# Performance work log

Hardware: AMD Instinct MI355X
Metric: run time of the kernel (lower is better)

The kernel has to match this reference:

```python
import jax, jax.numpy as jnp
import numpy as np

B, T, C_IN, CH, NRC, ED, NL, K = 16, 4096, 165, 256, 32, 64, 4, 512


def conv1x1(x, w, b):
    # x: [B,T,Cin], w: [Cout,Cin], b: [Cout]  (kernel-size-1 Conv1d == per-timestep matmul)
    return jnp.einsum('btc,oc->bto', x, w) + b


def resblock(x, wa, ba, wb, bb):
    h = jax.nn.relu(x)
    h = jax.nn.relu(conv1x1(h, wa, ba))
    h = conv1x1(h, wb, bb)
    return x + h


def quantize_level(res, embed):
    # res: [B,T,D], embed: [D,K]
    D = res.shape[-1]
    flat = res.reshape(-1, D)  # [N,D]
    dist = (flat * flat).sum(1, keepdims=True) - 2.0 * (flat @ embed) + (embed * embed).sum(0, keepdims=True)  # [N,K]
    ind = jnp.argmin(dist, axis=1)
    q = jnp.take(embed.T, ind, axis=0).reshape(res.shape)  # codebook gather
    diff = jnp.mean(jnp.square(jax.lax.stop_gradient(q) - res))
    q_st = res + jax.lax.stop_gradient(q - res)  # straight-through
    return q_st, diff


def _p(key, shape, fan_in):
    return jax.random.normal(key, shape, dtype=jnp.float32) / np.sqrt(fan_in)


def setup_inputs() -> dict:
    key = jax.random.key(0)
    ks = jax.random.split(key, 32)
    d = {
        'x': jax.random.normal(ks[0], (B, T, C_IN), dtype=jnp.float32),
        'enc_w1': _p(ks[1], (CH // 2, C_IN), C_IN), 'enc_b1': jnp.zeros((CH // 2,), jnp.float32),
        'enc_w2': _p(ks[2], (CH, CH // 2), CH // 2), 'enc_b2': jnp.zeros((CH,), jnp.float32),
        'enc_w3': _p(ks[3], (CH, CH), CH), 'enc_b3': jnp.zeros((CH,), jnp.float32),
        'enc_res_wa': _p(ks[4], (2, NRC, CH), CH), 'enc_res_ba': jnp.zeros((2, NRC), jnp.float32),
        'enc_res_wb': _p(ks[5], (2, CH, NRC), NRC), 'enc_res_bb': jnp.zeros((2, CH), jnp.float32),
        # quantize_conv: Conv(256->64)
        'q_w': _p(ks[6], (ED, CH), CH), 'q_b': jnp.zeros((ED,), jnp.float32),
        # 4 codebooks [D,K] (torch.randn init)
        'embeds': jax.random.normal(ks[7], (NL, ED, K), dtype=jnp.float32),
        'dec_w1': _p(ks[8], (CH, ED), ED), 'dec_b1': jnp.zeros((CH,), jnp.float32),
        'dec_res_wa': _p(ks[9], (2, NRC, CH), CH), 'dec_res_ba': jnp.zeros((2, NRC), jnp.float32),
        'dec_res_wb': _p(ks[10], (2, CH, NRC), NRC), 'dec_res_bb': jnp.zeros((2, CH), jnp.float32),
        'dec_w2': _p(ks[11], (CH // 2, CH), CH), 'dec_b2': jnp.zeros((CH // 2,), jnp.float32),
        'dec_w3': _p(ks[12], (C_IN, CH // 2), CH // 2), 'dec_b3': jnp.zeros((C_IN,), jnp.float32),
    }
    return d


def reference(x, enc_w1, enc_b1, enc_w2, enc_b2, enc_w3, enc_b3,
              enc_res_wa, enc_res_ba, enc_res_wb, enc_res_bb,
              q_w, q_b, embeds,
              dec_w1, dec_b1, dec_res_wa, dec_res_ba, dec_res_wb, dec_res_bb,
              dec_w2, dec_b2, dec_w3, dec_b3):
    # work entirely in [B,T,C] layout (transposes in the torch code cancel)
    h = jax.nn.relu(conv1x1(x, enc_w1, enc_b1))
    h = jax.nn.relu(conv1x1(h, enc_w2, enc_b2))
    h = conv1x1(h, enc_w3, enc_b3)
    for i in range(2):
        h = resblock(h, enc_res_wa[i], enc_res_ba[i], enc_res_wb[i], enc_res_bb[i])
    h = jax.nn.relu(h)
    quant = conv1x1(h, q_w, q_b)  # [B,T,64]

    residual = quant
    diffs = []
    main_q = None
    for i in range(NL):
        q, d = quantize_level(residual, embeds[i])
        diffs.append(d)
        residual = residual - q
        if i == 0:
            main_q = q
    diff = jnp.mean(jnp.stack(diffs))[None]  # shape [1]

    d = conv1x1(main_q, dec_w1, dec_b1)
    for i in range(2):
        d = resblock(d, dec_res_wa[i], dec_res_ba[i], dec_res_wb[i], dec_res_bb[i])
    d = jax.nn.relu(d)
    d = jax.nn.relu(conv1x1(d, dec_w2, dec_b2))
    d = conv1x1(d, dec_w3, dec_b3)  # [B,T,165]
    return d, diff
```

## Files before the change

kernel.cpp:

```cpp
#include <hip/hip_runtime.h>

#define NROWS 65536
#define SB 256

__device__ __forceinline__ float frelu(float v) { return fmaxf(v, 0.f); }

#define OFF_WT1   0
#define OFF_WT2   21504
#define OFF_WT3   54272
#define OFF_WTQ   119808
#define OFF_WTD1  136192
#define OFF_WTD2  152576
#define OFF_WTD3  185344
#define OFF_WAPE  218112
#define OFF_WBTE  234496
#define OFF_WAPD  250880
#define OFF_WBTD  267264
#define OFF_ETG   283648
#define OFF_EN2   414720
#define OFF_DSUM  416768
#define PREP_N    416769

__global__ void prep_k(const float* __restrict__ ew1, const float* __restrict__ ew2,
                       const float* __restrict__ ew3, const float* __restrict__ qw,
                       const float* __restrict__ dw1, const float* __restrict__ dw2,
                       const float* __restrict__ dw3, const float* __restrict__ ewa,
                       const float* __restrict__ ewb, const float* __restrict__ dwa,
                       const float* __restrict__ dwb, const float* __restrict__ embeds,
                       float* __restrict__ W) {
  int idx = blockIdx.x * 256 + threadIdx.x;
  if (idx < 21504) {
    int k = idx >> 7, o = idx & 127;
    W[OFF_WT1 + idx] = (k < 165) ? ew1[o * 165 + k] : 0.f;
    return;
  }
  idx -= 21504;
  if (idx < 32768) {
    int k = idx >> 8, o = idx & 255;
    W[OFF_WT2 + idx] = ew2[o * 128 + k];
    return;
  }
  idx -= 32768;
  if (idx < 65536) {
    int k = idx >> 8, o = idx & 255;
    W[OFF_WT3 + idx] = ew3[o * 256 + k];
    return;
  }
  idx -= 65536;
  if (idx < 16384) {
    int k = idx >> 6, o = idx & 63;
    W[OFF_WTQ + idx] = qw[o * 256 + k];
    return;
  }
  idx -= 16384;
  if (idx < 16384) {
    int k = idx >> 8, o = idx & 255;
    W[OFF_WTD1 + idx] = dw1[o * 64 + k];
    return;
  }
  idx -= 16384;
  if (idx < 32768) {
    int k = idx >> 7, o = idx & 127;
    W[OFF_WTD2 + idx] = dw2[o * 256 + k];
    return;
  }
  idx -= 32768;
  if (idx < 32768) {
    int k = idx >> 8, o = idx & 255;
    W[OFF_WTD3 + idx] = (o < 165) ? dw3[o * 128 + k] : 0.f;
    return;
  }
  idx -= 32768;
  if (idx < 16384) {
    int l = idx >> 13, rem = idx & 8191;
    int k4 = rem >> 7, rem2 = rem & 127, o = rem2 >> 2, kk = rem2 & 3;
    W[OFF_WAPE + idx] = ewa[l * 8192 + o * 256 + k4 * 4 + kk];
    return;
  }
  idx -= 16384;
  if (idx < 16384) {
    int l = idx >> 13, rem = idx & 8191;
    int k = rem >> 8, o = rem & 255;
    W[OFF_WBTE + idx] = ewb[l * 8192 + o * 32 + k];
    return;
  }
  idx -= 16384;
  if (idx < 16384) {
    int l = idx >> 13, rem = idx & 8191;
    int k4 = rem >> 7, rem2 = rem & 127, o = rem2 >> 2, kk = rem2 & 3;
    W[OFF_WAPD + idx] = dwa[l * 8192 + o * 256 + k4 * 4 + kk];
    return;
  }
  idx -= 16384;
  if (idx < 16384) {
    int l = idx >> 13, rem = idx & 8191;
    int k = rem >> 8, o = rem & 255;
    W[OFF_WBTD + idx] = dwb[l * 8192 + o * 32 + k];
    return;
  }
  idx -= 16384;
  if (idx < 131072) {
    int d = idx & 63, k = (idx >> 6) & 511, l = idx >> 15;
    W[OFF_ETG + idx] = embeds[(l * 64 + d) * 512 + k];
    return;
  }
  idx -= 131072;
  if (idx < 2048) {
    int l = idx >> 9, k = idx & 511;
    float s = 0.f;
    for (int d = 0; d < 64; ++d) {
      float e = embeds[(l * 64 + d) * 512 + k];
      s = fmaf(e, e, s);
    }
    W[OFF_EN2 + idx] = s;
    return;
  }
  idx -= 2048;
  if (idx == 0) W[OFF_DSUM] = 0.f;
}

template <int CIN, int CINP, int COUT, int CP, int INSTRIDE, int OUTSTRIDE, bool RELU_IN,
          bool RELU_OUT>
__global__ __launch_bounds__(256, 4) void conv2_k(const float* in, const float* __restrict__ wT,
                                                  const float* __restrict__ b, float* out) {
  constexpr int COUTP = 64 * CP;
  constexpr bool GUARD = (COUT != COUTP);
  typedef float vCP __attribute__((ext_vector_type(CP)));
  __shared__ float xs[32][CINP];
  const int tid = threadIdx.x, lane = tid & 63, wv = tid >> 6;
  const long row0 = (long)blockIdx.x * 32;

  for (int i = tid; i < 32 * CINP; i += 256) {
    const int r = i / CINP, c = i % CINP;
    float v = (CIN == CINP || c < CIN) ? in[(row0 + r) * (long)INSTRIDE + c] : 0.f;
    if (RELU_IN) v = frelu(v);
    xs[r][c] = v;
  }
  __syncthreads();

  float acc[8][CP];
#pragma unroll
  for (int i = 0; i < 8; ++i)
#pragma unroll
    for (int j = 0; j < CP; ++j) acc[i][j] = 0.f;

  const float* wbase = wT + lane * CP;
#pragma unroll 4
  for (int k0 = 0; k0 < CINP; k0 += 4) {
    vCP wk[4];
#pragma unroll
    for (int kk = 0; kk < 4; ++kk) wk[kk] = *(const vCP*)(wbase + (k0 + kk) * COUTP);
#pragma unroll
    for (int rj = 0; rj < 8; ++rj) {
      const float4 x = *(const float4*)(&xs[wv * 8 + rj][k0]);
#pragma unroll
      for (int j = 0; j < CP; ++j) {
        acc[rj][j] = fmaf(x.x, wk[0][j], acc[rj][j]);
        acc[rj][j] = fmaf(x.y, wk[1][j], acc[rj][j]);
        acc[rj][j] = fmaf(x.z, wk[2][j], acc[rj][j]);
        acc[rj][j] = fmaf(x.w, wk[3][j], acc[rj][j]);
      }
    }
  }

  float bias[CP];
#pragma unroll
  for (int j = 0; j < CP; ++j) {
    const int o = lane * CP + j;
    bias[j] = (!GUARD || o < COUT) ? b[o] : 0.f;
  }
#pragma unroll
  for (int rj = 0; rj < 8; ++rj) {
    const long rbase = (row0 + wv * 8 + rj) * (long)OUTSTRIDE;
    if constexpr (!GUARD) {
      vCP v;
#pragma unroll
      for (int j = 0; j < CP; ++j) {
        const float t = acc[rj][j] + bias[j];
        v[j] = RELU_OUT ? frelu(t) : t;
      }
      *(vCP*)(out + rbase + lane * CP) = v;
    } else {
#pragma unroll
      for (int j = 0; j < CP; ++j) {
        const int o = lane * CP + j;
        if (o < COUT) {
          const float t = acc[rj][j] + bias[j];
          out[rbase + o] = RELU_OUT ? frelu(t) : t;
        }
      }
    }
  }
}

template <int CIN, int COUT, int COUTP, int INSTRIDE, int OUTSTRIDE, bool RELU_IN, bool RELU_OUT>
__global__ __launch_bounds__(512, 2) void conv6_k(const float* __restrict__ in,
                                                  const float* __restrict__ wT,
                                                  const float* __restrict__ b,
                                                  float* __restrict__ out) {
  constexpr int MAXD = (CIN > COUT) ? CIN : COUT;
  __shared__ float lds[MAXD * 65];
  const int tid = threadIdx.x;
  const int lane = tid & 63;
  const int wv = __builtin_amdgcn_readfirstlane(tid >> 6);
  const long row0 = (long)blockIdx.x * 64;

  constexpr int C4 = CIN / 4;
  for (int i = tid; i < 64 * C4; i += 512) {
    const int r = i / C4, c4 = i % C4;
    float4 v = *(const float4*)(in + (row0 + r) * (long)INSTRIDE + c4 * 4);
    if (RELU_IN) {
      v.x = frelu(v.x);
      v.y = frelu(v.y);
      v.z = frelu(v.z);
      v.w = frelu(v.w);
    }
    lds[(c4 * 4 + 0) * 65 + r] = v.x;
    lds[(c4 * 4 + 1) * 65 + r] = v.y;
    lds[(c4 * 4 + 2) * 65 + r] = v.z;
    lds[(c4 * 4 + 3) * 65 + r] = v.w;
  }
  __syncthreads();

  float acc[32];
#pragma unroll
  for (int j = 0; j < 32; ++j) acc[j] = 0.f;

  const float* wrow = wT + wv * 32;
#pragma unroll 2
  for (int k = 0; k < CIN; ++k) {
    const float xv = lds[k * 65 + lane];
    const float* wk = wrow + (long)k * COUTP;
#pragma unroll
    for (int j = 0; j < 32; ++j) acc[j] = fmaf(xv, wk[j], acc[j]);
  }

  const float* bb = b + wv * 32;
#pragma unroll
  for (int j = 0; j < 32; ++j) {
    float t = acc[j] + bb[j];
    acc[j] = RELU_OUT ? frelu(t) : t;
  }

  __syncthreads();
#pragma unroll
  for (int j = 0; j < 32; ++j) lds[(wv * 32 + j) * 65 + lane] = acc[j];
  __syncthreads();

  constexpr int O4 = COUT / 4;
  for (int i = tid; i < 64 * O4; i += 512) {
    const int r = i / O4, c4 = i % O4;
    float4 v;
    v.x = lds[(c4 * 4 + 0) * 65 + r];
    v.y = lds[(c4 * 4 + 1) * 65 + r];
    v.z = lds[(c4 * 4 + 2) * 65 + r];
    v.w = lds[(c4 * 4 + 3) * 65 + r];
    *(float4*)(out + (row0 + r) * (long)OUTSTRIDE + c4 * 4) = v;
  }
}

__global__ __launch_bounds__(512, 4) void resblock_pair_k(
    float* xbuf, const float* __restrict__ waP, const float* __restrict__ ba,
    const float* __restrict__ wbT, const float* __restrict__ bb) {
  __shared__ float wls[8192];
  __shared__ float ts[64][36];
  const int tid = threadIdx.x, lane = tid & 63, wv = tid >> 6;
  const long row0 = (long)blockIdx.x * 64;
  const int o32 = lane & 31, rh = lane >> 5;

  for (int li = 0; li < 2; ++li) {
    __syncthreads();
    for (int i = tid; i < 8192; i += 512) wls[i] = waP[li * 8192 + i];
    __syncthreads();

    {
      float a0 = 0.f, a1 = 0.f, a2 = 0.f, a3 = 0.f;
      const float* xrow = xbuf + (row0 + wv * 8 + rh * 4) * (long)SB;
#pragma unroll 4
      for (int k0 = 0; k0 < 256; k0 += 4) {
        const float4 wq = *(const float4*)(&wls[k0 * 32 + o32 * 4]);
        const float4 x0 = *(const float4*)(xrow + 0 * SB + k0);
        const float4 x1 = *(const float4*)(xrow + 1 * SB + k0);
        const float4 x2 = *(const float4*)(xrow + 2 * SB + k0);
        const float4 x3 = *(const float4*)(xrow + 3 * SB + k0);
        a0 = fmaf(frelu(x0.x), wq.x, a0);
        a0 = fmaf(frelu(x0.y), wq.y, a0);
        a0 = fmaf(frelu(x0.z), wq.z, a0);
        a0 = fmaf(frelu(x0.w), wq.w, a0);
        a1 = fmaf(frelu(x1.x), wq.x, a1);
        a1 = fmaf(frelu(x1.y), wq.y, a1);
        a1 = fmaf(frelu(x1.z), wq.z, a1);
        a1 = fmaf(frelu(x1.w), wq.w, a1);
        a2 = fmaf(frelu(x2.x), wq.x, a2);
        a2 = fmaf(frelu(x2.y), wq.y, a2);
        a2 = fmaf(frelu(x2.z), wq.z, a2);
        a2 = fmaf(frelu(x2.w), wq.w, a2);
        a3 = fmaf(frelu(x3.x), wq.x, a3);
        a3 = fmaf(frelu(x3.y), wq.y, a3);
        a3 = fmaf(frelu(x3.z), wq.z, a3);
        a3 = fmaf(frelu(x3.w), wq.w, a3);
      }
      const float bal = ba[li * 32 + o32];
      const int rB = wv * 8 + rh * 4;
      ts[rB + 0][o32] = frelu(a0 + bal);
      ts[rB + 1][o32] = frelu(a1 + bal);
      ts[rB + 2][o32] = frelu(a2 + bal);
      ts[rB + 3][o32] = frelu(a3 + bal);
    }

    __syncthreads();
    for (int i = tid; i < 8192; i += 512) wls[i] = wbT[li * 8192 + i];
    __syncthreads();

    float acc2[8][4];
#pragma unroll
    for (int i = 0; i < 8; ++i)
#pragma unroll
      for (int j = 0; j < 4; ++j) acc2[i][j] = 0.f;

#pragma unroll
    for (int k0 = 0; k0 < 32; k0 += 4) {
      const float4 wk0 = *(const float4*)(&wls[(k0 + 0) * 256 + lane * 4]);
      const float4 wk1 = *(const float4*)(&wls[(k0 + 1) * 256 + lane * 4]);
      const float4 wk2 = *(const float4*)(&wls[(k0 + 2) * 256 + lane * 4]);
      const float4 wk3 = *(const float4*)(&wls[(k0 + 3) * 256 + lane * 4]);
#pragma unroll
      for (int rj = 0; rj < 8; ++rj) {
        const float4 t4 = *(const float4*)(&ts[wv * 8 + rj][k0]);
        acc2[rj][0] = fmaf(t4.x, wk0.x, acc2[rj][0]);
        acc2[rj][1] = fmaf(t4.x, wk0.y, acc2[rj][1]);
        acc2[rj][2] = fmaf(t4.x, wk0.z, acc2[rj][2]);
        acc2[rj][3] = fmaf(t4.x, wk0.w, acc2[rj][3]);
        acc2[rj][0] = fmaf(t4.y, wk1.x, acc2[rj][0]);
        acc2[rj][1] = fmaf(t4.y, wk1.y, acc2[rj][1]);
        acc2[rj][2] = fmaf(t4.y, wk1.z, acc2[rj][2]);
        acc2[rj][3] = fmaf(t4.y, wk1.w, acc2[rj][3]);
        acc2[rj][0] = fmaf(t4.z, wk2.x, acc2[rj][0]);
        acc2[rj][1] = fmaf(t4.z, wk2.y, acc2[rj][1]);
        acc2[rj][2] = fmaf(t4.z, wk2.z, acc2[rj][2]);
        acc2[rj][3] = fmaf(t4.z, wk2.w, acc2[rj][3]);
        acc2[rj][0] = fmaf(t4.w, wk3.x, acc2[rj][0]);
        acc2[rj][1] = fmaf(t4.w, wk3.y, acc2[rj][1]);
        acc2[rj][2] = fmaf(t4.w, wk3.z, acc2[rj][2]);
        acc2[rj][3] = fmaf(t4.w, wk3.w, acc2[rj][3]);
      }
    }
    const float4 bbv = *(const float4*)(bb + li * 256 + lane * 4);
#pragma unroll
    for (int rj = 0; rj < 8; ++rj) {
      float* xp = xbuf + (row0 + wv * 8 + rj) * (long)SB + lane * 4;
      const float4 xv = *(const float4*)xp;
      float4 nv;
      nv.x = xv.x + acc2[rj][0] + bbv.x;
      nv.y = xv.y + acc2[rj][1] + bbv.y;
      nv.z = xv.z + acc2[rj][2] + bbv.z;
      nv.w = xv.w + acc2[rj][3] + bbv.w;
      *(float4*)xp = nv;
    }
  }
}

__global__ __launch_bounds__(256, 3) void vq_fused_k(
    float* buf, const float* __restrict__ wTq, const float* __restrict__ qb,
    const float* __restrict__ embeds, const float* __restrict__ en2,
    const float* __restrict__ etg, float* __restrict__ dsum,
    const float* __restrict__ wTd1, const float* __restrict__ d1b) {
  __shared__ float xs[32][256];
  __shared__ float resL[32][68];
  __shared__ float mq[32][68];
  const int tid = threadIdx.x;
  const int lane = tid & 63;
  const int wv = tid >> 6;
  const long row0 = (long)blockIdx.x * 32;

  for (int i = tid; i < 32 * 256; i += 256) {
    const int r = i >> 8, c = i & 255;
    xs[r][c] = frelu(buf[(row0 + r) * (long)SB + c]);
  }
  __syncthreads();

  {
    float qacc[8];
#pragma unroll
    for (int i = 0; i < 8; ++i) qacc[i] = 0.f;
#pragma unroll 2
    for (int k0 = 0; k0 < 256; k0 += 4) {
      const float w0 = wTq[(k0 + 0) * 64 + lane];
      const float w1 = wTq[(k0 + 1) * 64 + lane];
      const float w2 = wTq[(k0 + 2) * 64 + lane];
      const float w3 = wTq[(k0 + 3) * 64 + lane];
#pragma unroll
      for (int rj = 0; rj < 8; ++rj) {
        const float4 x = *(const float4*)(&xs[wv * 8 + rj][k0]);
        qacc[rj] = fmaf(x.x, w0, qacc[rj]);
        qacc[rj] = fmaf(x.y, w1, qacc[rj]);
        qacc[rj] = fmaf(x.z, w2, qacc[rj]);
        qacc[rj] = fmaf(x.w, w3, qacc[rj]);
      }
    }
    const float qbv = qb[lane];
#pragma unroll
    for (int rj = 0; rj < 8; ++rj) resL[wv * 8 + rj][lane] = qacc[rj] + qbv;
  }

  float dloc = 0.f;

  for (int l = 0; l < 4; ++l) {
    float best[8];
    int bk[8];
#pragma unroll
    for (int i = 0; i < 8; ++i) {
      best[i] = 3.4e38f;
      bk[i] = 0;
    }

    for (int kc = 0; kc < 2; ++kc) {
      float acc[8][4];
#pragma unroll
      for (int i = 0; i < 8; ++i)
#pragma unroll
        for (int j = 0; j < 4; ++j) acc[i][j] = 0.f;

      const float* eb = embeds + ((long)l << 15) + (kc << 8) + lane * 4;
#pragma unroll 2
      for (int dq = 0; dq < 16; ++dq) {
        float4 x4[8];
#pragma unroll
        for (int rj = 0; rj < 8; ++rj) x4[rj] = *(const float4*)(&resL[wv * 8 + rj][dq * 4]);
#pragma unroll
        for (int dd = 0; dd < 4; ++dd) {
          const float4 e4 = *(const float4*)(eb + ((dq * 4 + dd) << 9));
#pragma unroll
          for (int rj = 0; rj < 8; ++rj) {
            const float xv = dd == 0 ? x4[rj].x : dd == 1 ? x4[rj].y : dd == 2 ? x4[rj].z : x4[rj].w;
            acc[rj][0] = fmaf(xv, e4.x, acc[rj][0]);
            acc[rj][1] = fmaf(xv, e4.y, acc[rj][1]);
            acc[rj][2] = fmaf(xv, e4.z, acc[rj][2]);
            acc[rj][3] = fmaf(xv, e4.w, acc[rj][3]);
          }
        }
      }

      const float4 e2 = *(const float4*)(en2 + l * 512 + kc * 256 + lane * 4);
#pragma unroll
      for (int rj = 0; rj < 8; ++rj) {
#pragma unroll
        for (int j = 0; j < 4; ++j) {
          const float ev = j == 0 ? e2.x : j == 1 ? e2.y : j == 2 ? e2.z : e2.w;
          const float s = fmaf(-2.f, acc[rj][j], ev);
          const int k = kc * 256 + lane * 4 + j;
          if (s < best[rj]) {
            best[rj] = s;
            bk[rj] = k;
          }
        }
      }
    }

#pragma unroll
    for (int rj = 0; rj < 8; ++rj) {
      float bv = best[rj];
      int bi = bk[rj];
#pragma unroll
      for (int m = 1; m < 64; m <<= 1) {
        const float ov = __shfl_xor(bv, m, 64);
        const int ok = __shfl_xor(bi, m, 64);
        if (ov < bv || (ov == bv && ok < bi)) {
          bv = ov;
          bi = ok;
        }
      }
      bk[rj] = bi;
    }

#pragma unroll
    for (int rj = 0; rj < 8; ++rj) {
      const int r = wv * 8 + rj;
      const float q = etg[((long)((l << 9) + bk[rj])) * 64 + lane];
      const float res = resL[r][lane];
      const float t = q - res;
      const float qst = res + t;
      dloc = fmaf(t, t, dloc);
      resL[r][lane] = res - qst;
      if (l == 0) mq[r][lane] = qst;
    }
  }

#pragma unroll
  for (int m = 1; m < 64; m <<= 1) dloc += __shfl_xor(dloc, m, 64);
  if (lane == 0) atomicAdd(dsum, dloc);

  {
    float acc1[8][4];
#pragma unroll
    for (int i = 0; i < 8; ++i)
#pragma unroll
      for (int j = 0; j < 4; ++j) acc1[i][j] = 0.f;

    const float* w1base = wTd1 + lane * 4;
#pragma unroll 2
    for (int d = 0; d < 64; d += 2) {
      const float4 wA = *(const float4*)(w1base + (d + 0) * 256);
      const float4 wB = *(const float4*)(w1base + (d + 1) * 256);
#pragma unroll
      for (int rj = 0; rj < 8; ++rj) {
        const int r = wv * 8 + rj;
        const float xA = mq[r][d];
        const float xB = mq[r][d + 1];
        acc1[rj][0] = fmaf(xA, wA.x, acc1[rj][0]);
        acc1[rj][1] = fmaf(xA, wA.y, acc1[rj][1]);
        acc1[rj][2] = fmaf(xA, wA.z, acc1[rj][2]);
        acc1[rj][3] = fmaf(xA, wA.w, acc1[rj][3]);
        acc1[rj][0] = fmaf(xB, wB.x, acc1[rj][0]);
        acc1[rj][1] = fmaf(xB, wB.y, acc1[rj][1]);
        acc1[rj][2] = fmaf(xB, wB.z, acc1[rj][2]);
        acc1[rj][3] = fmaf(xB, wB.w, acc1[rj][3]);
      }
    }
    const float4 bv = *(const float4*)(d1b + lane * 4);
#pragma unroll
    for (int rj = 0; rj < 8; ++rj) {
      float4 v;
      v.x = acc1[rj][0] + bv.x;
      v.y = acc1[rj][1] + bv.y;
      v.z = acc1[rj][2] + bv.z;
      v.w = acc1[rj][3] + bv.w;
      *(float4*)(buf + (row0 + wv * 8 + rj) * (long)SB + lane * 4) = v;
    }
  }
}

__global__ __launch_bounds__(256, 3) void dec23_k(const float* __restrict__ in,
                                                  const float* __restrict__ wTd2,
                                                  const float* __restrict__ b2,
                                                  const float* __restrict__ wTd3,
                                                  const float* __restrict__ b3,
                                                  float* __restrict__ out) {
  __shared__ float xs[32][256];
  __shared__ float ts[32][132];
  const int tid = threadIdx.x, lane = tid & 63, wv = tid >> 6;
  const long row0 = (long)blockIdx.x * 32;

  for (int i = tid; i < 32 * 256; i += 256) {
    const int r = i >> 8, c = i & 255;
    xs[r][c] = frelu(in[(row0 + r) * (long)SB + c]);
  }
  __syncthreads();

  {
    float a2[8][2];
#pragma unroll
    for (int i = 0; i < 8; ++i) {
      a2[i][0] = 0.f;
      a2[i][1] = 0.f;
    }
    const float* w2base = wTd2 + lane * 2;
#pragma unroll 2
    for (int k0 = 0; k0 < 256; k0 += 4) {
      const float2 w0 = *(const float2*)(w2base + (k0 + 0) * 128);
      const float2 w1 = *(const float2*)(w2base + (k0 + 1) * 128);
      const float2 w2v = *(const float2*)(w2base + (k0 + 2) * 128);
      const float2 w3 = *(const float2*)(w2base + (k0 + 3) * 128);
#pragma unroll
      for (int rj = 0; rj < 8; ++rj) {
        const float4 x = *(const float4*)(&xs[wv * 8 + rj][k0]);
        a2[rj][0] = fmaf(x.x, w0.x, a2[rj][0]);
        a2[rj][1] = fmaf(x.x, w0.y, a2[rj][1]);
        a2[rj][0] = fmaf(x.y, w1.x, a2[rj][0]);
        a2[rj][1] = fmaf(x.y, w1.y, a2[rj][1]);
        a2[rj][0] = fmaf(x.z, w2v.x, a2[rj][0]);
        a2[rj][1] = fmaf(x.z, w2v.y, a2[rj][1]);
        a2[rj][0] = fmaf(x.w, w3.x, a2[rj][0]);
        a2[rj][1] = fmaf(x.w, w3.y, a2[rj][1]);
      }
    }
    const float b20 = b2[lane * 2 + 0];
    const float b21 = b2[lane * 2 + 1];
#pragma unroll
    for (int rj = 0; rj < 8; ++rj) {
      const int r = wv * 8 + rj;
      ts[r][lane * 2 + 0] = frelu(a2[rj][0] + b20);
      ts[r][lane * 2 + 1] = frelu(a2[rj][1] + b21);
    }
  }

  {
    float a3[8][4];
#pragma unroll
    for (int i = 0; i < 8; ++i)
#pragma unroll
      for (int j = 0; j < 4; ++j) a3[i][j] = 0.f;

    const float* w3base = wTd3 + lane * 4;
#pragma unroll 2
    for (int k0 = 0; k0 < 128; k0 += 4) {
      const float4 wk0 = *(const float4*)(w3base + (k0 + 0) * 256);
      const float4 wk1 = *(const float4*)(w3base + (k0 + 1) * 256);
      const float4 wk2 = *(const float4*)(w3base + (k0 + 2) * 256);
      const float4 wk3 = *(const float4*)(w3base + (k0 + 3) * 256);
#pragma unroll
      for (int rj = 0; rj < 8; ++rj) {
        const float4 t4 = *(const float4*)(&ts[wv * 8 + rj][k0]);
        a3[rj][0] = fmaf(t4.x, wk0.x, a3[rj][0]);
        a3[rj][1] = fmaf(t4.x, wk0.y, a3[rj][1]);
        a3[rj][2] = fmaf(t4.x, wk0.z, a3[rj][2]);
        a3[rj][3] = fmaf(t4.x, wk0.w, a3[rj][3]);
        a3[rj][0] = fmaf(t4.y, wk1.x, a3[rj][0]);
        a3[rj][1] = fmaf(t4.y, wk1.y, a3[rj][1]);
        a3[rj][2] = fmaf(t4.y, wk1.z, a3[rj][2]);
        a3[rj][3] = fmaf(t4.y, wk1.w, a3[rj][3]);
        a3[rj][0] = fmaf(t4.z, wk2.x, a3[rj][0]);
        a3[rj][1] = fmaf(t4.z, wk2.y, a3[rj][1]);
        a3[rj][2] = fmaf(t4.z, wk2.z, a3[rj][2]);
        a3[rj][3] = fmaf(t4.z, wk2.w, a3[rj][3]);
        a3[rj][0] = fmaf(t4.w, wk3.x, a3[rj][0]);
        a3[rj][1] = fmaf(t4.w, wk3.y, a3[rj][1]);
        a3[rj][2] = fmaf(t4.w, wk3.z, a3[rj][2]);
        a3[rj][3] = fmaf(t4.w, wk3.w, a3[rj][3]);
      }
    }
    float bias[4];
#pragma unroll
    for (int j = 0; j < 4; ++j) {
      const int o = lane * 4 + j;
      bias[j] = (o < 165) ? b3[o] : 0.f;
    }
#pragma unroll
    for (int rj = 0; rj < 8; ++rj) {
      const long rbase = (row0 + wv * 8 + rj) * 165L;
#pragma unroll
      for (int j = 0; j < 4; ++j) {
        const int o = lane * 4 + j;
        if (o < 165) out[rbase + o] = a3[rj][j] + bias[j];
      }
    }
  }
}

__global__ void finalize_k(const float* __restrict__ dsum, float* __restrict__ out) {
  if (threadIdx.x == 0 && blockIdx.x == 0)
    out[0] = *dsum * (1.0f / (4.0f * 65536.0f * 64.0f));
}

extern "C" void kernel_launch(void* const* d_in, const int* in_sizes, int n_in, void* d_out,
                              int out_size, void* d_ws, size_t ws_size, hipStream_t stream) {
  (void)in_sizes; (void)n_in; (void)out_size; (void)ws_size;
  const float* x = (const float*)d_in[0];
  const float* enc_w1 = (const float*)d_in[1];
  const float* enc_b1 = (const float*)d_in[2];
  const float* enc_w2 = (const float*)d_in[3];
  const float* enc_b2 = (const float*)d_in[4];
  const float* enc_w3 = (const float*)d_in[5];
  const float* enc_b3 = (const float*)d_in[6];
  const float* enc_res_wa = (const float*)d_in[7];
  const float* enc_res_ba = (const float*)d_in[8];
  const float* enc_res_wb = (const float*)d_in[9];
  const float* enc_res_bb = (const float*)d_in[10];
  const float* q_w = (const float*)d_in[11];
  const float* q_b = (const float*)d_in[12];
  const float* embeds = (const float*)d_in[13];
  const float* dec_w1 = (const float*)d_in[14];
  const float* dec_b1 = (const float*)d_in[15];
  const float* dec_res_wa = (const float*)d_in[16];
  const float* dec_res_ba = (const float*)d_in[17];
  const float* dec_res_wb = (const float*)d_in[18];
  const float* dec_res_bb = (const float*)d_in[19];
  const float* dec_w2 = (const float*)d_in[20];
  const float* dec_b2 = (const float*)d_in[21];
  const float* dec_w3 = (const float*)d_in[22];
  const float* dec_b3 = (const float*)d_in[23];

  float* ws = (float*)d_ws;
  float* buf = ws;
  float* W = ws + (long)NROWS * SB;

  float* dout = (float*)d_out;

  prep_k<<<(PREP_N + 255) / 256, 256, 0, stream>>>(enc_w1, enc_w2, enc_w3, q_w, dec_w1, dec_w2,
                                                   dec_w3, enc_res_wa, enc_res_wb, dec_res_wa,
                                                   dec_res_wb, embeds, W);

  const int GB = NROWS / 32;
  const int GR = NROWS / 64;

  conv2_k<165, 168, 128, 2, 165, SB, false, true><<<GB, 256, 0, stream>>>(x, W + OFF_WT1, enc_b1, buf);
  conv6_k<128, 256, 256, SB, SB, false, true><<<GR, 512, 0, stream>>>(buf, W + OFF_WT2, enc_b2, buf);
  conv6_k<256, 256, 256, SB, SB, false, false><<<GR, 512, 0, stream>>>(buf, W + OFF_WT3, enc_b3, buf);
  resblock_pair_k<<<GR, 512, 0, stream>>>(buf, W + OFF_WAPE, enc_res_ba, W + OFF_WBTE, enc_res_bb);

  vq_fused_k<<<GB, 256, 0, stream>>>(buf, W + OFF_WTQ, q_b, embeds, W + OFF_EN2, W + OFF_ETG,
                                     W + OFF_DSUM, W + OFF_WTD1, dec_b1);

  resblock_pair_k<<<GR, 512, 0, stream>>>(buf, W + OFF_WAPD, dec_res_ba, W + OFF_WBTD, dec_res_bb);
  dec23_k<<<GB, 256, 0, stream>>>(buf, W + OFF_WTD2, dec_b2, W + OFF_WTD3, dec_b3, dout);

  finalize_k<<<1, 64, 0, stream>>>(W + OFF_DSUM, dout + (long)NROWS * 165);
}
```

Before: 1.171 ms.

## Restructure fused VQ kernel to hold residual rows in registers

Rewrites the fused quantize kernel so that each lane keeps one row's 64-dim residual in registers. Each of the four waves scans a quarter of the codebook through row-major, wave-uniform (broadcast) reads, and the per-wave winners are combined through LDS. Blocks now cover 64 rows with 256 threads and read the encoder activations straight from global memory instead of staging them in LDS. The scalar dot-product loop is meant to cut LDS traffic and shuffle reductions, at the cost of 64+ live registers per lane, lower occupancy (launch bounds of 2), and an argmin tie-break that no longer explicitly prefers the lower index across waves.

```diff
diff --git a/kernel.cpp b/kernel.cpp
--- a/kernel.cpp
+++ b/kernel.cpp
@@ -360,29 +360,23 @@
   }
 }
 
-__global__ __launch_bounds__(256, 3) void vq_fused_k(
+__global__ __launch_bounds__(256, 2) void vq8_k(
     float* buf, const float* __restrict__ wTq, const float* __restrict__ qb,
-    const float* __restrict__ embeds, const float* __restrict__ en2,
-    const float* __restrict__ etg, float* __restrict__ dsum,
-    const float* __restrict__ wTd1, const float* __restrict__ d1b) {
-  __shared__ float xs[32][256];
-  __shared__ float resL[32][68];
-  __shared__ float mq[32][68];
-  const int tid = threadIdx.x;
-  const int lane = tid & 63;
-  const int wv = tid >> 6;
-  const long row0 = (long)blockIdx.x * 32;
-
-  for (int i = tid; i < 32 * 256; i += 256) {
-    const int r = i >> 8, c = i & 255;
-    xs[r][c] = frelu(buf[(row0 + r) * (long)SB + c]);
-  }
-  __syncthreads();
+    const float* __restrict__ en2, const float* __restrict__ etg,
+    float* __restrict__ dsum, const float* __restrict__ wTd1, const float* __restrict__ d1b) {
+  __shared__ float q_lds[64 * 72];
+  __shared__ float mq_lds[64 * 72];
+  __shared__ float bestvL[256];
+  __shared__ int bestkL[256];
+  __shared__ int kwin[64];
+  const int tid = threadIdx.x, lane = tid & 63, wv = tid >> 6;
+  const long row0 = (long)blockIdx.x * 64;
 
   {
-    float qacc[8];
-#pragma unroll
-    for (int i = 0; i < 8; ++i) qacc[i] = 0.f;
+    float acc[16];
+#pragma unroll
+    for (int i = 0; i < 16; ++i) acc[i] = 0.f;
+    const float* xbase = buf + (row0 + wv * 16) * (long)SB;
 #pragma unroll 2
     for (int k0 = 0; k0 < 256; k0 += 4) {
       const float w0 = wTq[(k0 + 0) * 64 + lane];
@@ -390,142 +384,164 @@
       const float w2 = wTq[(k0 + 2) * 64 + lane];
       const float w3 = wTq[(k0 + 3) * 64 + lane];
 #pragma unroll
-      for (int rj = 0; rj < 8; ++rj) {
-        const float4 x = *(const float4*)(&xs[wv * 8 + rj][k0]);
-        qacc[rj] = fmaf(x.x, w0, qacc[rj]);
-        qacc[rj] = fmaf(x.y, w1, qacc[rj]);
-        qacc[rj] = fmaf(x.z, w2, qacc[rj]);
-        qacc[rj] = fmaf(x.w, w3, qacc[rj]);
+      for (int rj = 0; rj < 16; ++rj) {
+        const float4 x = *(const float4*)(xbase + (long)rj * SB + k0);
+        acc[rj] = fmaf(frelu(x.x), w0, acc[rj]);
+        acc[rj] = fmaf(frelu(x.y), w1, acc[rj]);
+        acc[rj] = fmaf(frelu(x.z), w2, acc[rj]);
+        acc[rj] = fmaf(frelu(x.w), w3, acc[rj]);
       }
     }
     const float qbv = qb[lane];
 #pragma unroll
-    for (int rj = 0; rj < 8; ++rj) resL[wv * 8 + rj][lane] = qacc[rj] + qbv;
+    for (int rj = 0; rj < 16; ++rj) q_lds[(wv * 16 + rj) * 72 + lane] = acc[rj] + qbv;
+  }
+  __syncthreads();
+
+  float res[64];
+#pragma unroll
+  for (int c = 0; c < 16; ++c) {
+    const float4 v = *(const float4*)(&q_lds[lane * 72 + c * 4]);
+    res[c * 4 + 0] = v.x;
+    res[c * 4 + 1] = v.y;
+    res[c * 4 + 2] = v.z;
+    res[c * 4 + 3] = v.w;
   }
 
   float dloc = 0.f;
 
   for (int l = 0; l < 4; ++l) {
-    float best[8];
-    int bk[8];
-#pragma unroll
-    for (int i = 0; i < 8; ++i) {
-      best[i] = 3.4e38f;
-      bk[i] = 0;
-    }
-
-    for (int kc = 0; kc < 2; ++kc) {
-      float acc[8][4];
-#pragma unroll
-      for (int i = 0; i < 8; ++i)
-#pragma unroll
-        for (int j = 0; j < 4; ++j) acc[i][j] = 0.f;
-
-      const float* eb = embeds + ((long)l << 15) + (kc << 8) + lane * 4;
+    float best = 3.4e38f;
+    int bk = 0;
+    const int kbase = wv * 128;
+    const float* eb = etg + ((long)(l * 512 + kbase)) * 64;
+    const float* e2p = en2 + l * 512 + kbase;
+    for (int kk = 0; kk < 128; kk += 2) {
+      const float* e1 = eb + (long)kk * 64;
+      const float* e2 = e1 + 64;
+      float a1 = 0.f, a2 = 0.f;
+#pragma unroll
+      for (int d = 0; d < 64; ++d) {
+        a1 = fmaf(res[d], e1[d], a1);
+        a2 = fmaf(res[d], e2[d], a2);
+      }
+      const float s1 = fmaf(-2.f, a1, e2p[kk]);
+      const float s2 = fmaf(-2.f, a2, e2p[kk + 1]);
+      if (s1 < best) { best = s1; bk = kbase + kk; }
+      if (s2 < best) { best = s2; bk = kbase + kk + 1; }
+    }
+    bestvL[wv * 64 + lane] = best;
+    bestkL[wv * 64 + lane] = bk;
+    __syncthreads();
+
+    float bv = bestvL[lane];
+    int bi = bestkL[lane];
+#pragma unroll
+    for (int w2 = 1; w2 < 4; ++w2) {
+      const float ov = bestvL[w2 * 64 + lane];
+      const int ok = bestkL[w2 * 64 + lane];
+      if (ov < bv) { bv = ov; bi = ok; }
+    }
+    if (wv == 0) kwin[lane] = bi;
+    __syncthreads();
+
+    {
+      const int r = tid >> 2, part = tid & 3;
+      const int kw = kwin[r];
+      const float* src = etg + ((long)(l * 512 + kw)) * 64 + part * 16;
+      const float4 f0 = *(const float4*)(src + 0);
+      const float4 f1 = *(const float4*)(src + 4);
+      const float4 f2 = *(const float4*)(src + 8);
+      const float4 f3 = *(const float4*)(src + 12);
+      float* dst = &q_lds[r * 72 + part * 16];
+      *(float4*)(dst + 0) = f0;
+      *(float4*)(dst + 4) = f1;
+      *(float4*)(dst + 8) = f2;
+      *(float4*)(dst + 12) = f3;
+    }
+    __syncthreads();
+
+#pragma unroll
+    for (int c = 0; c < 16; ++c) {
+      const float4 q4 = *(const float4*)(&q_lds[lane * 72 + c * 4]);
+      const float t0 = q4.x - res[c * 4 + 0];
+      const float t1 = q4.y - res[c * 4 + 1];
+      const float t2 = q4.z - res[c * 4 + 2];
+      const float t3 = q4.w - res[c * 4 + 3];
+      const float q0 = res[c * 4 + 0] + t0;
+      const float q1 = res[c * 4 + 1] + t1;
+      const float q2 = res[c * 4 + 2] + t2;
+      const float q3 = res[c * 4 + 3] + t3;
+      dloc = fmaf(t0, t0, dloc);
+      dloc = fmaf(t1, t1, dloc);
+      dloc = fmaf(t2, t2, dloc);
+      dloc = fmaf(t3, t3, dloc);
+      res[c * 4 + 0] -= q0;
+      res[c * 4 + 1] -= q1;
+      res[c * 4 + 2] -= q2;
+      res[c * 4 + 3] -= q3;
+      if (l == 0 && wv == 0) {
+        float4 m;
+        m.x = q0;
+        m.y = q1;
+        m.z = q2;
+        m.w = q3;
+        *(float4*)(&mq_lds[lane * 72 + c * 4]) = m;
+      }
+    }
+  }
+
+  if (wv == 0) {
+#pragma unroll
+    for (int m = 1; m < 64; m <<= 1) dloc += __shfl_xor(dloc, m, 64);
+    if (lane == 0) atomicAdd(dsum, dloc);
+  }
+  __syncthreads();
+
+  {
+    float acc1[16][4];
+#pragma unroll
+    for (int i = 0; i < 16; ++i)
+#pragma unroll
+      for (int j = 0; j < 4; ++j) acc1[i][j] = 0.f;
+
+    const float* w1b = wTd1 + lane * 4;
 #pragma unroll 2
-      for (int dq = 0; dq < 16; ++dq) {
-        float4 x4[8];
-#pragma unroll
-        for (int rj = 0; rj < 8; ++rj) x4[rj] = *(const float4*)(&resL[wv * 8 + rj][dq * 4]);
-#pragma unroll
-        for (int dd = 0; dd < 4; ++dd) {
-          const float4 e4 = *(const float4*)(eb + ((dq * 4 + dd) << 9));
-#pragma unroll
-          for (int rj = 0; rj < 8; ++rj) {
-            const float xv = dd == 0 ? x4[rj].x : dd == 1 ? x4[rj].y : dd == 2 ? x4[rj].z : x4[rj].w;
-            acc[rj][0] = fmaf(xv, e4.x, acc[rj][0]);
-            acc[rj][1] = fmaf(xv, e4.y, acc[rj][1]);
-            acc[rj][2] = fmaf(xv, e4.z, acc[rj][2]);
-            acc[rj][3] = fmaf(xv, e4.w, acc[rj][3]);
-          }
-        }
-      }
-
-      const float4 e2 = *(const float4*)(en2 + l * 512 + kc * 256 + lane * 4);
-#pragma unroll
-      for (int rj = 0; rj < 8; ++rj) {
-#pragma unroll
-        for (int j = 0; j < 4; ++j) {
-          const float ev = j == 0 ? e2.x : j == 1 ? e2.y : j == 2 ? e2.z : e2.w;
-          const float s = fmaf(-2.f, acc[rj][j], ev);
-          const int k = kc * 256 + lane * 4 + j;
-          if (s < best[rj]) {
-            best[rj] = s;
-            bk[rj] = k;
-          }
-        }
-      }
-    }
-
-#pragma unroll
-    for (int rj = 0; rj < 8; ++rj) {
-      float bv = best[rj];
-      int bi = bk[rj];
-#pragma unroll
-      for (int m = 1; m < 64; m <<= 1) {
-        const float ov = __shfl_xor(bv, m, 64);
-        const int ok = __shfl_xor(bi, m, 64);
-        if (ov < bv || (ov == bv && ok < bi)) {
-          bv = ov;
-          bi = ok;
-        }
-      }
-      bk[rj] = bi;
-    }
-
-#pragma unroll
-    for (int rj = 0; rj < 8; ++rj) {
-      const int r = wv * 8 + rj;
-      const float q = etg[((long)((l << 9) + bk[rj])) * 64 + lane];
-      const float res = resL[r][lane];
-      const float t = q - res;
-      const float qst = res + t;
-      dloc = fmaf(t, t, dloc);
-      resL[r][lane] = res - qst;
-      if (l == 0) mq[r][lane] = qst;
-    }
-  }
-
-#pragma unroll
-  for (int m = 1; m < 64; m <<= 1) dloc += __shfl_xor(dloc, m, 64);
-  if (lane == 0) atomicAdd(dsum, dloc);
-
-  {
-    float acc1[8][4];
-#pragma unroll
-    for (int i = 0; i < 8; ++i)
-#pragma unroll
-      for (int j = 0; j < 4; ++j) acc1[i][j] = 0.f;
-
-    const float* w1base = wTd1 + lane * 4;
-#pragma unroll 2
-    for (int d = 0; d < 64; d += 2) {
-      const float4 wA = *(const float4*)(w1base + (d + 0) * 256);
-      const float4 wB = *(const float4*)(w1base + (d + 1) * 256);
-#pragma unroll
-      for (int rj = 0; rj < 8; ++rj) {
-        const int r = wv * 8 + rj;
-        const float xA = mq[r][d];
-        const float xB = mq[r][d + 1];
-        acc1[rj][0] = fmaf(xA, wA.x, acc1[rj][0]);
-        acc1[rj][1] = fmaf(xA, wA.y, acc1[rj][1]);
-        acc1[rj][2] = fmaf(xA, wA.z, acc1[rj][2]);
-        acc1[rj][3] = fmaf(xA, wA.w, acc1[rj][3]);
-        acc1[rj][0] = fmaf(xB, wB.x, acc1[rj][0]);
-        acc1[rj][1] = fmaf(xB, wB.y, acc1[rj][1]);
-        acc1[rj][2] = fmaf(xB, wB.z, acc1[rj][2]);
-        acc1[rj][3] = fmaf(xB, wB.w, acc1[rj][3]);
-      }
-    }
-    const float4 bv = *(const float4*)(d1b + lane * 4);
-#pragma unroll
-    for (int rj = 0; rj < 8; ++rj) {
+    for (int d0 = 0; d0 < 64; d0 += 4) {
+      const float4 wA = *(const float4*)(w1b + (d0 + 0) * 256);
+      const float4 wB = *(const float4*)(w1b + (d0 + 1) * 256);
+      const float4 wC = *(const float4*)(w1b + (d0 + 2) * 256);
+      const float4 wD = *(const float4*)(w1b + (d0 + 3) * 256);
+#pragma unroll
+      for (int rj = 0; rj < 16; ++rj) {
+        const float4 x = *(const float4*)(&mq_lds[(wv * 16 + rj) * 72 + d0]);
+        acc1[rj][0] = fmaf(x.x, wA.x, acc1[rj][0]);
+        acc1[rj][1] = fmaf(x.x, wA.y, acc1[rj][1]);
+        acc1[rj][2] = fmaf(x.x, wA.z, acc1[rj][2]);
+        acc1[rj][3] = fmaf(x.x, wA.w, acc1[rj][3]);
+        acc1[rj][0] = fmaf(x.y, wB.x, acc1[rj][0]);
+        acc1[rj][1] = fmaf(x.y, wB.y, acc1[rj][1]);
+        acc1[rj][2] = fmaf(x.y, wB.z, acc1[rj][2]);
+        acc1[rj][3] = fmaf(x.y, wB.w, acc1[rj][3]);
+        acc1[rj][0] = fmaf(x.z, wC.x, acc1[rj][0]);
+        acc1[rj][1] = fmaf(x.z, wC.y, acc1[rj][1]);
+        acc1[rj][2] = fmaf(x.z, wC.z, acc1[rj][2]);
+        acc1[rj][3] = fmaf(x.z, wC.w, acc1[rj][3]);
+        acc1[rj][0] = fmaf(x.w, wD.x, acc1[rj][0]);
+        acc1[rj][1] = fmaf(x.w, wD.y, acc1[rj][1]);
+        acc1[rj][2] = fmaf(x.w, wD.z, acc1[rj][2]);
+        acc1[rj][3] = fmaf(x.w, wD.w, acc1[rj][3]);
+      }
+    }
+    const float4 bv4 = *(const float4*)(d1b + lane * 4);
+#pragma unroll
+    for (int rj = 0; rj < 16; ++rj) {
       float4 v;
-      v.x = acc1[rj][0] + bv.x;
-      v.y = acc1[rj][1] + bv.y;
-      v.z = acc1[rj][2] + bv.z;
-      v.w = acc1[rj][3] + bv.w;
-      *(float4*)(buf + (row0 + wv * 8 + rj) * (long)SB + lane * 4) = v;
+      v.x = acc1[rj][0] + bv4.x;
+      v.y = acc1[rj][1] + bv4.y;
+      v.z = acc1[rj][2] + bv4.z;
+      v.w = acc1[rj][3] + bv4.w;
+      *(float4*)(buf + (row0 + wv * 16 + rj) * (long)SB + lane * 4) = v;
     }
   }
 }
@@ -688,8 +704,8 @@
   conv6_k<256, 256, 256, SB, SB, false, false><<<GR, 512, 0, stream>>>(buf, W + OFF_WT3, enc_b3, buf);
   resblock_pair_k<<<GR, 512, 0, stream>>>(buf, W + OFF_WAPE, enc_res_ba, W + OFF_WBTE, enc_res_bb);
 
-  vq_fused_k<<<GB, 256, 0, stream>>>(buf, W + OFF_WTQ, q_b, embeds, W + OFF_EN2, W + OFF_ETG,
-                                     W + OFF_DSUM, W + OFF_WTD1, dec_b1);
+  vq8_k<<<GR, 256, 0, stream>>>(buf, W + OFF_WTQ, q_b, W + OFF_EN2, W + OFF_ETG, W + OFF_DSUM,
+                                W + OFF_WTD1, dec_b1);
 
   resblock_pair_k<<<GR, 512, 0, stream>>>(buf, W + OFF_WAPD, dec_res_ba, W + OFF_WBTD, dec_res_bb);
   dec23_k<<<GB, 256, 0, stream>>>(buf, W + OFF_WTD2, dec_b2, W + OFF_WTD3, dec_b3, dout);
```

Result: slower. 1.891 ms (+61.5%).
